# Kernel optimization log

Hardware: AMD Instinct MI355X
Metric: run time of the kernel (lower is better)

## Reference

```python
import jax, jax.numpy as jnp
import numpy as np

N_NODES = 358
NODE_DIM = 64
EMBED_DIM = 96
G_HEADS = 4
TOPK = 10
B = 8
P = 72
MHA_HEADS = 4


def _ln(x, g, b, eps=1e-5):
    m = x.mean(-1, keepdims=True)
    v = jnp.var(x, axis=-1, keepdims=True)
    return (x - m) * jax.lax.rsqrt(v + eps) * g + b


def _gelu(x):
    return jax.nn.gelu(x, approximate=False)


def _topk_sparsify(a, k):
    # top-k mask per row over last dim, then row-renormalize (matches torch version)
    shp = a.shape
    n = shp[-1]
    flat = a.reshape(-1, n)
    _, idx = jax.lax.top_k(flat, k)
    rows = jnp.arange(flat.shape[0])[:, None]
    mask = jnp.zeros_like(flat).at[rows, idx].set(1.0)
    sp = flat * mask
    sp = sp / (sp.sum(-1, keepdims=True) + 1e-8)
    return sp.reshape(shp)


def _forward(patch_features, se2, le1, le2, ge1, ge2, temperature, in_proj_w, in_proj_b, out_proj_w, out_proj_b, tn_g, tn_b, de_w1, de_b1, de_ln1_g, de_ln1_b, de_w2, de_b2, de_ln2_g, de_ln2_b, pos_enc, gnn1_w, gnn1_b, gnn1_g, gnn1_beta, gnn2_w, gnn2_b, gnn2_g, gnn2_beta, gf_w, gf_b, ee_w1, ee_b1, ee_ln_g, ee_ln_b, ee_w2, ee_b2, ee_w3, ee_b3):
    Bn, N, Pn, D = patch_features.shape
    H = temperature.shape[0]
    Hl = H // 2
    # --- static multi-head graphs (local + global) ---
    ladj = jax.nn.relu(jnp.einsum('hnd,hdm->hnm', le1, le2))
    ladj = jax.nn.softmax(ladj / jnp.clip(temperature[:Hl] * 2.0, 0.1, 5.0)[:, None, None], axis=-1)
    gadj = jax.nn.relu(jnp.einsum('hnd,hdm->hnm', ge1, ge2))
    gadj = jax.nn.softmax(gadj / jnp.clip(temperature[Hl:] * 0.5, 0.1, 2.0)[:, None, None], axis=-1)
    static_adjs = jnp.concatenate([ladj, gadj], axis=0)  # (H,N,N)
    # --- dynamic graphs from patch features ---
    pr = patch_features.reshape(Bn * N, Pn, D)
    x = pr + pos_enc[:, :Pn, :]
    # torch nn.MultiheadAttention self-attention (eval mode, no dropout)
    qkv = x @ in_proj_w.T + in_proj_b
    q, k, v = jnp.split(qkv, 3, axis=-1)
    hd = D // MHA_HEADS

    def split_heads(t):
        return t.reshape(Bn * N, Pn, MHA_HEADS, hd).transpose(0, 2, 1, 3)

    q, k, v = split_heads(q), split_heads(k), split_heads(v)
    attn = jax.nn.softmax(jnp.einsum('bhqd,bhkd->bhqk', q, k) * (1.0 / float(np.sqrt(hd))), axis=-1)
    att = jnp.einsum('bhqk,bhkd->bhqd', attn, v).transpose(0, 2, 1, 3).reshape(Bn * N, Pn, D)
    att = att @ out_proj_w.T + out_proj_b
    imp = jax.nn.softmax(att.mean(-1), axis=1)  # (BN,P) patch importance
    node_repr = _ln((att * imp[..., None]).sum(1) + pr.mean(1), tn_g, tn_b).reshape(Bn, N, D)
    # dynamic encoder: Linear -> LN -> GELU -> Linear -> LN
    de = _ln(_gelu(_ln(node_repr @ de_w1.T + de_b1, de_ln1_g, de_ln1_b)) @ de_w2.T + de_b2, de_ln2_g, de_ln2_b)
    # two GNN refinement layers: bmm -> softmax -> bmm -> (Linear,LN,GELU) + residual
    for w, b_, g_, bt in ((gnn1_w, gnn1_b, gnn1_g, gnn1_beta), (gnn2_w, gnn2_b, gnn2_g, gnn2_beta)):
        sims = jax.nn.softmax(jnp.einsum('bnd,bmd->bnm', de, de) / 0.2, axis=2)
        agg = jnp.einsum('bnm,bmd->bnd', sims, de)
        de = _gelu(_ln(agg @ w.T + b_, g_, bt)) + de
    dyn = jax.nn.relu(jnp.einsum('bnd,hdm->bhnm', de, se2))
    dynamic_adjs = jax.nn.softmax(dyn / jnp.clip(temperature, 0.1, 2.0)[None, :, None, None], axis=3)
    # --- top-k sparsification ---
    static_adjs = _topk_sparsify(static_adjs, TOPK)
    dynamic_adjs = _topk_sparsify(dynamic_adjs, TOPK)
    # --- static/dynamic fusion ---
    fw = jax.nn.sigmoid(patch_features.mean(2) @ gf_w.T + gf_b)  # (B,N,H)
    fw = fw.transpose(0, 2, 1)[..., None]  # (B,H,N,1) broadcasts over last N
    fused = (1.0 - fw) * static_adjs[None] + fw * dynamic_adjs  # (B,H,N,N)
    # --- edge encoder over head dim ---
    mh = fused.transpose(0, 2, 3, 1)  # (B,N,N,H)
    h1 = _gelu(_ln(mh @ ee_w1.T + ee_b1, ee_ln_g, ee_ln_b))
    h2 = _gelu(h1 @ ee_w2.T + ee_b2)
    ew = (h2 @ ee_w3.T + ee_b3)[..., 0]  # (B,N,N)
    final_adjs = jax.nn.sigmoid(ew) * fused.mean(1)
    return final_adjs, static_adjs, dynamic_adjs


def setup_inputs() -> dict:
    key = jax.random.key(0)
    ks = iter(jax.random.split(key, 64))
    D, nd, H = EMBED_DIM, NODE_DIM, G_HEADS
    Hl = H // 2
    Hg = H - Hl

    def rn(shape, s=0.05):
        return jax.random.normal(next(ks), shape, jnp.float32) * s

    z = lambda *s: jnp.zeros(s, jnp.float32)
    o = lambda *s: jnp.ones(s, jnp.float32)
    return dict(
        patch_features=jax.random.normal(next(ks), (B, N_NODES, P, D), jnp.float32),
        se2=rn((H, nd, N_NODES)),
        le1=rn((Hl, N_NODES, nd // 2)), le2=rn((Hl, nd // 2, N_NODES)),
        ge1=rn((Hg, N_NODES, nd)), ge2=rn((Hg, nd, N_NODES)),
        temperature=jnp.full((H,), 0.5, jnp.float32),
        in_proj_w=rn((3 * D, D)), in_proj_b=z(3 * D),
        out_proj_w=rn((D, D)), out_proj_b=z(D),
        tn_g=o(D), tn_b=z(D),
        de_w1=rn((2 * nd, D)), de_b1=z(2 * nd), de_ln1_g=o(2 * nd), de_ln1_b=z(2 * nd),
        de_w2=rn((nd, 2 * nd)), de_b2=z(nd), de_ln2_g=o(nd), de_ln2_b=z(nd),
        pos_enc=rn((1, 72, D), 1.0),
        gnn1_w=rn((nd, nd)), gnn1_b=z(nd), gnn1_g=o(nd), gnn1_beta=z(nd),
        gnn2_w=rn((nd, nd)), gnn2_b=z(nd), gnn2_g=o(nd), gnn2_beta=z(nd),
        gf_w=rn((H, D)), gf_b=z(H),
        ee_w1=rn((4 * H, H)), ee_b1=z(4 * H), ee_ln_g=o(4 * H), ee_ln_b=z(4 * H),
        ee_w2=rn((2 * H, 4 * H)), ee_b2=z(2 * H),
        ee_w3=rn((1, 2 * H)), ee_b3=z(1),
    )


def reference(patch_features, se2, le1, le2, ge1, ge2, temperature, in_proj_w, in_proj_b, out_proj_w, out_proj_b, tn_g, tn_b, de_w1, de_b1, de_ln1_g, de_ln1_b, de_w2, de_b2, de_ln2_g, de_ln2_b, pos_enc, gnn1_w, gnn1_b, gnn1_g, gnn1_beta, gnn2_w, gnn2_b, gnn2_g, gnn2_beta, gf_w, gf_b, ee_w1, ee_b1, ee_ln_g, ee_ln_b, ee_w2, ee_b2, ee_w3, ee_b3):
    return _forward(patch_features, se2, le1, le2, ge1, ge2, temperature, in_proj_w, in_proj_b, out_proj_w, out_proj_b, tn_g, tn_b, de_w1, de_b1, de_ln1_g, de_ln1_b, de_w2, de_b2, de_ln2_g, de_ln2_b, pos_enc, gnn1_w, gnn1_b, gnn1_g, gnn1_beta, gnn2_w, gnn2_b, gnn2_g, gnn2_beta, gf_w, gf_b, ee_w1, ee_b1, ee_ln_g, ee_ln_b, ee_w2, ee_b2, ee_w3, ee_b3)
```

## Files before the change

kernel.cpp:

```cpp
#include <hip/hip_runtime.h>
#include <math.h>

#define NNODES 358
#define NN2 (358*358)
#define DIM 96
#define PP 72
#define ND 64
#define NB 8
#define NH 4
#define SEQ (NB*NNODES)

#define WS_WT2   0
#define WS_WBAR  27648
#define WS_BBAR  27744
#define WS_POSB  27748
#define WS_PRM   27848
#define WS_DEA   302792
#define WS_DEB   486088

__device__ __forceinline__ float gelu_f(float y) {
  return 0.5f*y*(1.0f+erff(y*0.70710678118654752440f));
}

__device__ __forceinline__ void wave_topk_row(const float* __restrict__ lgr,
                                              float* __restrict__ orow)
{
  int lane = threadIdx.x & 63;
  float vals[6];
  #pragma unroll
  for (int j = 0; j < 6; ++j) {
    int m = lane + 64*j;
    vals[j] = (m < NNODES) ? lgr[m] : -1e30f;
  }
  float mx = vals[0];
  #pragma unroll
  for (int j = 1; j < 6; ++j) mx = fmaxf(mx, vals[j]);
  #pragma unroll
  for (int o = 32; o; o >>= 1) mx = fmaxf(mx, __shfl_xor(mx, o, 64));
  float M = mx;
  float ls = 0.0f;
  #pragma unroll
  for (int j = 0; j < 6; ++j) ls += __expf(vals[j] - M);
  #pragma unroll
  for (int o = 32; o; o >>= 1) ls += __shfl_xor(ls, o, 64);
  float invS = 1.0f/ls;
  float outv[6] = {0.f, 0.f, 0.f, 0.f, 0.f, 0.f};
  float ss = 0.0f;
  for (int it = 0; it < 10; ++it) {
    float v = -1e30f; int idx = 0x7fffffff;
    #pragma unroll
    for (int j = 0; j < 6; ++j) {
      if (vals[j] > v) { v = vals[j]; idx = lane + 64*j; }
    }
    #pragma unroll
    for (int o = 1; o < 64; o <<= 1) {
      float ov = __shfl_xor(v, o, 64);
      int oi = __shfl_xor(idx, o, 64);
      if (ov > v || (ov == v && oi < idx)) { v = ov; idx = oi; }
    }
    ss += __expf(v - M);
    #pragma unroll
    for (int j = 0; j < 6; ++j)
      if (lane + 64*j == idx) { outv[j] = __expf(v - M); vals[j] = -1e30f; }
  }
  float dn = 1.0f/(ss*invS + 1e-8f);
  #pragma unroll
  for (int j = 0; j < 6; ++j) {
    int m = lane + 64*j;
    if (m < NNODES) orow[m] = outv[j]*invS*dn;
  }
}

__global__ void k0_setup(const float* __restrict__ wi, const float* __restrict__ wo,
                         const float* __restrict__ bo, const float* __restrict__ pos,
                         float* __restrict__ ws)
{
  int t = threadIdx.x;
  for (int idx = t; idx < 4*96*72; idx += 256) {
    int h = idx / (96*72);
    int r = idx - h*96*72;
    int k = r / 72;
    int gc = r - k*72;
    int g = gc / 24, c = gc - g*24;
    ws[WS_WT2 + idx] = wi[(size_t)(g*96 + h*24 + c)*96 + k];
  }
  if (t < 96) {
    float sm = 0.0f;
    for (int d = 0; d < 96; ++d) sm += wo[d*96 + t];
    ws[WS_WBAR + t] = sm*(1.0f/96.0f);
    float ps = 0.0f;
    for (int p = 0; p < PP; ++p) ps += pos[p*96 + t];
    ws[WS_POSB + t] = ps*(1.0f/72.0f);
  }
  if (t == 0) {
    float sm = 0.0f;
    for (int d = 0; d < 96; ++d) sm += bo[d];
    ws[WS_BBAR] = sm*(1.0f/96.0f);
  }
}

#define K1_RPB 4
#define K1_BPH 90

__global__ void __launch_bounds__(256)
k1_static4(const float* __restrict__ le1, const float* __restrict__ le2,
           const float* __restrict__ ge1, const float* __restrict__ ge2,
           const float* __restrict__ temp, float* __restrict__ outstat)
{
  __shared__ float e1s[K1_RPB][64];
  __shared__ float lg[K1_RPB][NNODES];
  int blk = blockIdx.x, t = threadIdx.x;
  int h = blk / K1_BPH;
  int n0 = (blk - h*K1_BPH)*K1_RPB;
  int nrows = NNODES - n0; if (nrows > K1_RPB) nrows = K1_RPB;
  int kd; const float* e2p; float tau;
  if (h < 2) {
    kd = 32;
    e2p = le2 + (size_t)h*32*NNODES;
    tau = fminf(fmaxf(temp[h]*2.0f, 0.1f), 5.0f);
  } else {
    kd = 64;
    e2p = ge2 + (size_t)(h-2)*64*NNODES;
    tau = fminf(fmaxf(temp[h]*0.5f, 0.1f), 2.0f);
  }
  {
    int r = t >> 6, k = t & 63;
    float v = 0.0f;
    if (r < nrows && k < kd)
      v = (h < 2) ? le1[((size_t)h*NNODES + n0 + r)*32 + k]
                  : ge1[((size_t)(h-2)*NNODES + n0 + r)*64 + k];
    e1s[r][k] = v;
  }
  __syncthreads();
  float itau = 1.0f/tau;
  for (int m = t; m < NNODES; m += 256) {
    float s0=0.f, s1=0.f, s2=0.f, s3=0.f;
    for (int k = 0; k < kd; ++k) {
      float ev = e2p[k*NNODES + m];
      s0 += e1s[0][k]*ev;
      s1 += e1s[1][k]*ev;
      s2 += e1s[2][k]*ev;
      s3 += e1s[3][k]*ev;
    }
    lg[0][m] = fmaxf(s0, 0.0f)*itau;
    lg[1][m] = fmaxf(s1, 0.0f)*itau;
    lg[2][m] = fmaxf(s2, 0.0f)*itau;
    lg[3][m] = fmaxf(s3, 0.0f)*itau;
  }
  __syncthreads();
  int wv = t >> 6;
  if (wv < nrows)
    wave_topk_row(lg[wv], outstat + ((size_t)h*NNODES + n0 + wv)*NNODES);
}

#define A_XS    0
#define A_WH    7200
#define A_SS    7200
#define A_WB    7200
#define A_LIMP  7296
#define A_IMP   7368
#define A_WSUM  7440
#define A_NB    7536
#define A_NR    7632
#define A_H1    7728
#define A_G1    7856
#define A_H2    7984
#define A_PART  12672
#define A_PART2 13184
#define A_QH    14112
#define A_KT    16128
#define A_VT    17952
#define A_PRM   19776
#define A_TOT   19872

__global__ void __launch_bounds__(512, 4)
k2a_fused(const float* __restrict__ pf, const float* __restrict__ pos,
          const float* __restrict__ inb, float* __restrict__ ws,
          const float* __restrict__ wo, const float* __restrict__ bo,
          const float* __restrict__ tng, const float* __restrict__ tnb,
          const float* __restrict__ dw1, const float* __restrict__ db1,
          const float* __restrict__ dg1, const float* __restrict__ dlb1,
          const float* __restrict__ dw2, const float* __restrict__ db2,
          const float* __restrict__ dg2, const float* __restrict__ dlb2)
{
  __shared__ __align__(16) float L[A_TOT];
  int t = threadIdx.x;
  size_t s = blockIdx.x;
  const float* prp = pf + s*(PP*DIM);
  for (int idx = t; idx < 1728; idx += 512) {
    float4 v = ((const float4*)prp)[idx];
    float4 q = ((const float4*)pos)[idx];
    v.x += q.x; v.y += q.y; v.z += q.z; v.w += q.w;
    int p = idx / 24, e4 = idx - p*24;
    *(float4*)&L[A_XS + p*100 + e4*4] = v;
  }
  __syncthreads();
  if (t < DIM) {
    float sm = 0.0f;
    for (int p = 0; p < PP; ++p) sm += L[A_XS + p*100 + t];
    sm = sm*(1.0f/72.0f) - ws[WS_POSB + t];
    L[A_PRM + t] = sm;
    ws[WS_PRM + s*DIM + t] = sm;
  }
  const float SC = 0.20412414523193150f;
  float4 oreg0, oreg1, oreg2, oreg3;
  #pragma unroll
  for (int h = 0; h < NH; ++h) {
    __syncthreads();
    __builtin_amdgcn_sched_barrier(0);
    const float4* wsrc = (const float4*)(ws + WS_WT2 + (size_t)h*6912);
    for (int idx = t; idx < 1728; idx += 512)
      *(float4*)&L[A_WH + idx*4] = wsrc[idx];
    __builtin_amdgcn_sched_barrier(0);
    __syncthreads();
    if (t < 432) {
      int rt = t / 18, ct = t - rt*18;
      int p0 = rt*3, cc0 = ct*4;
      float acc[3][4];
      #pragma unroll
      for (int a = 0; a < 3; ++a)
        { acc[a][0]=0.f; acc[a][1]=0.f; acc[a][2]=0.f; acc[a][3]=0.f; }
      for (int k0 = 0; k0 < 96; k0 += 4) {
        float4 xv[3];
        #pragma unroll
        for (int a = 0; a < 3; ++a) xv[a] = *(const float4*)&L[A_XS + (p0+a)*100 + k0];
        float4 wv[4];
        #pragma unroll
        for (int kk = 0; kk < 4; ++kk) wv[kk] = *(const float4*)&L[A_WH + (k0+kk)*72 + cc0];
        #pragma unroll
        for (int kk = 0; kk < 4; ++kk) {
          #pragma unroll
          for (int a = 0; a < 3; ++a) {
            float xa = ((const float*)&xv[a])[kk];
            acc[a][0] += xa*wv[kk].x;
            acc[a][1] += xa*wv[kk].y;
            acc[a][2] += xa*wv[kk].z;
            acc[a][3] += xa*wv[kk].w;
          }
        }
      }
      int g = cc0 / 24;
      int ch = cc0 - g*24;
      #pragma unroll
      for (int c = 0; c < 4; ++c) {
        float bias = inb[g*96 + h*24 + ch + c];
        #pragma unroll
        for (int a = 0; a < 3; ++a) {
          float v = acc[a][c] + bias;
          int p = p0 + a;
          if (g == 0)      L[A_QH + p*28 + ch + c] = v*SC;
          else if (g == 1) L[A_KT + (ch+c)*76 + p] = v;
          else             L[A_VT + (ch+c)*76 + p] = v;
        }
      }
    }
    __syncthreads();
    for (int tile = t; tile < 648; tile += 512) {
      int pt2 = tile / 18, jt2 = tile - pt2*18;
      int p0 = pt2*2, j0 = jt2*4;
      float a0=0,a1=0,a2=0,a3=0, c0=0,c1=0,c2=0,c3=0;
      #pragma unroll
      for (int d0 = 0; d0 < 24; d0 += 4) {
        float4 q0 = *(const float4*)&L[A_QH + p0*28 + d0];
        float4 q1 = *(const float4*)&L[A_QH + (p0+1)*28 + d0];
        #pragma unroll
        for (int dd = 0; dd < 4; ++dd) {
          float4 kv = *(const float4*)&L[A_KT + (d0+dd)*76 + j0];
          float qa = ((const float*)&q0)[dd];
          float qb = ((const float*)&q1)[dd];
          a0 += qa*kv.x; a1 += qa*kv.y; a2 += qa*kv.z; a3 += qa*kv.w;
          c0 += qb*kv.x; c1 += qb*kv.y; c2 += qb*kv.z; c3 += qb*kv.w;
        }
      }
      *(float4*)&L[A_SS + p0*76 + j0]     = make_float4(a0,a1,a2,a3);
      *(float4*)&L[A_SS + (p0+1)*76 + j0] = make_float4(c0,c1,c2,c3);
    }
    __syncthreads();
    if (t < 288) {
      int r = t >> 2, sg = t & 3, j0 = sg*18;
      const float* row = &L[A_SS + r*76];
      float mx = row[j0];
      for (int j = j0+1; j < j0+18; ++j) mx = fmaxf(mx, row[j]);
      L[A_PART + t] = mx;
    }
    __syncthreads();
    if (t < 288) {
      int r = t >> 2, sg = t & 3, j0 = sg*18;
      int rb = r << 2;
      float M = fmaxf(fmaxf(L[A_PART+rb], L[A_PART+rb+1]),
                      fmaxf(L[A_PART+rb+2], L[A_PART+rb+3]));
      float* row = &L[A_SS + r*76];
      float sm = 0.0f;
      for (int j = j0; j < j0+18; ++j) { float e = __expf(row[j]-M); row[j] = e; sm += e; }
      L[A_PART2 + t] = sm;
    }
    __syncthreads();
    if (t < 432) {
      int p = t / 6, dt = t - (t/6)*6;
      int d0 = dt*4, rb = p << 2;
      float S4 = L[A_PART2+rb]+L[A_PART2+rb+1]+L[A_PART2+rb+2]+L[A_PART2+rb+3];
      float inv = 1.0f/S4;
      float a0=0,a1=0,a2=0,a3=0;
      for (int j0 = 0; j0 < 72; j0 += 4) {
        float4 pv = *(const float4*)&L[A_SS + p*76 + j0];
        float4 v0 = *(const float4*)&L[A_VT + (d0+0)*76 + j0];
        float4 v1 = *(const float4*)&L[A_VT + (d0+1)*76 + j0];
        float4 v2 = *(const float4*)&L[A_VT + (d0+2)*76 + j0];
        float4 v3 = *(const float4*)&L[A_VT + (d0+3)*76 + j0];
        a0 += pv.x*v0.x + pv.y*v0.y + pv.z*v0.z + pv.w*v0.w;
        a1 += pv.x*v1.x + pv.y*v1.y + pv.z*v1.z + pv.w*v1.w;
        a2 += pv.x*v2.x + pv.y*v2.y + pv.z*v2.z + pv.w*v2.w;
        a3 += pv.x*v3.x + pv.y*v3.y + pv.z*v3.z + pv.w*v3.w;
      }
      float4 ov = make_float4(a0*inv, a1*inv, a2*inv, a3*inv);
      if (h == 0)      oreg0 = ov;
      else if (h == 1) oreg1 = ov;
      else if (h == 2) oreg2 = ov;
      else             oreg3 = ov;
    }
  }
  __syncthreads();
  if (t < 432) {
    int p = t / 6, dt = t - (t/6)*6;
    int d0 = dt*4;
    *(float4*)&L[A_XS + p*100 +  0 + d0] = oreg0;
    *(float4*)&L[A_XS + p*100 + 24 + d0] = oreg1;
    *(float4*)&L[A_XS + p*100 + 48 + d0] = oreg2;
    *(float4*)&L[A_XS + p*100 + 72 + d0] = oreg3;
  }
  if (t < 96) L[A_WB + t] = ws[WS_WBAR + t];
  __syncthreads();
  if (t < 288) {
    int r = t >> 2, sg = t & 3, e0 = sg*24;
    float sm = 0.0f;
    for (int e = e0; e < e0+24; ++e) sm += L[A_XS + r*100 + e]*L[A_WB + e];
    L[A_PART + t] = sm;
  }
  __syncthreads();
  if (t < 72) {
    int rb = t << 2;
    L[A_LIMP + t] = L[A_PART+rb]+L[A_PART+rb+1]+L[A_PART+rb+2]+L[A_PART+rb+3]
                  + ws[WS_BBAR];
  }
  __syncthreads();
  if (t < 72) {
    float mx = L[A_LIMP];
    for (int j = 1; j < 72; ++j) mx = fmaxf(mx, L[A_LIMP+j]);
    float sm = 0.0f;
    for (int j = 0; j < 72; ++j) sm += __expf(L[A_LIMP+j]-mx);
    L[A_IMP + t] = __expf(L[A_LIMP+t]-mx)/sm;
  }
  __syncthreads();
  if (t < 384) {
    int c = t >> 2, sg = t & 3, p0 = sg*18;
    float sm = 0.0f;
    for (int p = p0; p < p0+18; ++p) sm += L[A_IMP+p]*L[A_XS + p*100 + c];
    L[A_PART + t] = sm;
  }
  __syncthreads();
  if (t < 96) {
    int rb = t << 2;
    L[A_WSUM + t] = L[A_PART+rb]+L[A_PART+rb+1]+L[A_PART+rb+2]+L[A_PART+rb+3];
  }
  __syncthreads();
  if (t < 384) {
    int c = t >> 2, sg = t & 3, e0 = sg*24;
    float sm = 0.0f;
    for (int e = e0; e < e0+24; ++e) sm += L[A_WSUM+e]*wo[c*96 + e];
    L[A_PART + t] = sm;
  }
  __syncthreads();
  if (t < 96) {
    int rb = t << 2;
    L[A_NB + t] = L[A_PART+rb]+L[A_PART+rb+1]+L[A_PART+rb+2]+L[A_PART+rb+3]
                + bo[t] + L[A_PRM + t];
  }
  __syncthreads();
  if (t < 96) {
    float mean = 0.0f;
    for (int e = 0; e < 96; ++e) mean += L[A_NB+e];
    mean *= (1.0f/96.0f);
    float var = 0.0f;
    for (int e = 0; e < 96; ++e) { float d = L[A_NB+e]-mean; var += d*d; }
    var *= (1.0f/96.0f);
    L[A_NR + t] = (L[A_NB+t]-mean)*rsqrtf(var+1e-5f)*tng[t] + tnb[t];
  }
  __syncthreads();
  {
    int c = t >> 2, sg = t & 3, k0 = sg*24;
    float sm = 0.0f;
    for (int k = k0; k < k0+24; ++k) sm += L[A_NR+k]*dw1[c*96 + k];
    L[A_PART + t] = sm;
  }
  __syncthreads();
  if (t < 128) {
    int rb = t << 2;
    L[A_H1 + t] = L[A_PART+rb]+L[A_PART+rb+1]+L[A_PART+rb+2]+L[A_PART+rb+3] + db1[t];
  }
  __syncthreads();
  if (t < 128) {
    float mean = 0.0f; for (int e = 0; e < 128; ++e) mean += L[A_H1+e];
    mean *= (1.0f/128.0f);
    float var = 0.0f; for (int e = 0; e < 128; ++e) { float d = L[A_H1+e]-mean; var += d*d; }
    var *= (1.0f/128.0f);
    float y = (L[A_H1+t]-mean)*rsqrtf(var+1e-5f)*dg1[t] + dlb1[t];
    L[A_G1 + t] = gelu_f(y);
  }
  __syncthreads();
  if (t < 256) {
    int c = t >> 2, sg = t & 3, k0 = sg*32;
    float sm = 0.0f;
    for (int k = k0; k < k0+32; ++k) sm += L[A_G1+k]*dw2[c*128 + k];
    L[A_PART + t] = sm;
  }
  __syncthreads();
  if (t < 64) {
    int rb = t << 2;
    L[A_H2 + t] = L[A_PART+rb]+L[A_PART+rb+1]+L[A_PART+rb+2]+L[A_PART+rb+3] + db2[t];
  }
  __syncthreads();
  if (t < 64) {
    float mean = 0.0f; for (int e = 0; e < 64; ++e) mean += L[A_H2+e];
    mean *= (1.0f/64.0f);
    float var = 0.0f; for (int e = 0; e < 64; ++e) { float d = L[A_H2+e]-mean; var += d*d; }
    var *= (1.0f/64.0f);
    ws[WS_DEA + s*ND + t] = (L[A_H2+t]-mean)*rsqrtf(var+1e-5f)*dg2[t] + dlb2[t];
  }
}

#define K4_RPB 4
#define K4_BPB 90

__global__ void __launch_bounds__(256)
k4_gnn(float* __restrict__ ws, int inoff, int outoff,
       const float* __restrict__ w, const float* __restrict__ bb,
       const float* __restrict__ g, const float* __restrict__ beta)
{
  __shared__ __align__(16) float nrow[K4_RPB][64];
  __shared__ float lg[K4_RPB][NNODES];
  __shared__ float pbl[K4_RPB][NNODES];
  __shared__ float aggp[4][K4_RPB][64];
  __shared__ float aggb[K4_RPB][64];
  __shared__ float prj[K4_RPB][64];
  int blk = blockIdx.x, t = threadIdx.x;
  int b = blk / K4_BPB;
  int n0 = (blk - b*K4_BPB)*K4_RPB;
  int nrows = NNODES - n0; if (nrows > K4_RPB) nrows = K4_RPB;
  {
    int r = t >> 6, d = t & 63;
    nrow[r][d] = (r < nrows)
      ? ws[inoff + ((size_t)(b*NNODES) + n0 + r)*ND + d] : 0.0f;
  }
  __syncthreads();
  const float* deb = ws + inoff + (size_t)b*NNODES*ND;
  for (int m = t; m < NNODES; m += 256) {
    const float* dr = deb + (size_t)m*ND;
    float s0=0.f, s1=0.f, s2=0.f, s3=0.f;
    #pragma unroll
    for (int d0 = 0; d0 < 64; d0 += 4) {
      float4 dv = *(const float4*)&dr[d0];
      float4 n0v = *(const float4*)&nrow[0][d0];
      float4 n1v = *(const float4*)&nrow[1][d0];
      float4 n2v = *(const float4*)&nrow[2][d0];
      float4 n3v = *(const float4*)&nrow[3][d0];
      s0 += dv.x*n0v.x + dv.y*n0v.y + dv.z*n0v.z + dv.w*n0v.w;
      s1 += dv.x*n1v.x + dv.y*n1v.y + dv.z*n1v.z + dv.w*n1v.w;
      s2 += dv.x*n2v.x + dv.y*n2v.y + dv.z*n2v.z + dv.w*n2v.w;
      s3 += dv.x*n3v.x + dv.y*n3v.y + dv.z*n3v.z + dv.w*n3v.w;
    }
    lg[0][m] = s0*5.0f;
    lg[1][m] = s1*5.0f;
    lg[2][m] = s2*5.0f;
    lg[3][m] = s3*5.0f;
  }
  __syncthreads();
  int wv = t >> 6, lane = t & 63;
  {
    const float* lgr = lg[wv];
    float vals[6];
    #pragma unroll
    for (int j = 0; j < 6; ++j) {
      int m = lane + 64*j;
      vals[j] = (m < NNODES) ? lgr[m] : -1e30f;
    }
    float mx = vals[0];
    #pragma unroll
    for (int j = 1; j < 6; ++j) mx = fmaxf(mx, vals[j]);
    #pragma unroll
    for (int o = 32; o; o >>= 1) mx = fmaxf(mx, __shfl_xor(mx, o, 64));
    float M = mx;
    float ls = 0.0f;
    #pragma unroll
    for (int j = 0; j < 6; ++j) ls += __expf(vals[j] - M);
    #pragma unroll
    for (int o = 32; o; o >>= 1) ls += __shfl_xor(ls, o, 64);
    float inv = 1.0f/ls;
    #pragma unroll
    for (int j = 0; j < 6; ++j) {
      int m = lane + 64*j;
      if (m < NNODES) pbl[wv][m] = __expf(vals[j] - M)*inv;
    }
  }
  __syncthreads();
  {
    int d = lane;
    float a0=0.f, a1=0.f, a2=0.f, a3=0.f;
    for (int m = wv; m < NNODES; m += 4) {
      float dv = deb[(size_t)m*ND + d];
      a0 += pbl[0][m]*dv;
      a1 += pbl[1][m]*dv;
      a2 += pbl[2][m]*dv;
      a3 += pbl[3][m]*dv;
    }
    aggp[wv][0][d] = a0;
    aggp[wv][1][d] = a1;
    aggp[wv][2][d] = a2;
    aggp[wv][3][d] = a3;
  }
  __syncthreads();
  {
    int r = t >> 6, d = t & 63;
    aggb[r][d] = aggp[0][r][d]+aggp[1][r][d]+aggp[2][r][d]+aggp[3][r][d];
  }
  __syncthreads();
  {
    int r = t >> 6, c = t & 63;
    float sm = 0.0f;
    for (int d = 0; d < 64; ++d) sm += aggb[r][d]*w[c*64 + d];
    prj[r][c] = sm + bb[c];
  }
  __syncthreads();
  {
    int r = t >> 6, c = t & 63;
    float mean = 0.0f; for (int e = 0; e < 64; ++e) mean += prj[r][e];
    mean *= (1.0f/64.0f);
    float var = 0.0f; for (int e = 0; e < 64; ++e) { float d = prj[r][e]-mean; var += d*d; }
    var *= (1.0f/64.0f);
    float y = (prj[r][c]-mean)*rsqrtf(var+1e-5f)*g[c] + beta[c];
    if (r < nrows)
      ws[outoff + ((size_t)(b*NNODES) + n0 + r)*ND + c] = gelu_f(y) + nrow[r][c];
  }
}

#define K5_RPB 4
#define K5_BPH 90

__global__ void __launch_bounds__(256)
k5_dyn4(const float* __restrict__ ws, const float* __restrict__ se2,
        const float* __restrict__ temp, float* __restrict__ outdyn)
{
  __shared__ float den[K5_RPB][64];
  __shared__ float lg[K5_RPB][NNODES];
  int blk = blockIdx.x, t = threadIdx.x;
  int bh = blk / K5_BPH;
  int n0 = (blk - bh*K5_BPH)*K5_RPB;
  int h = bh & 3, b = bh >> 2;
  int nrows = NNODES - n0; if (nrows > K5_RPB) nrows = K5_RPB;
  if (t < K5_RPB*64) {
    int r = t >> 6, d = t & 63;
    den[r][d] = (r < nrows)
      ? ws[WS_DEA + ((size_t)(b*NNODES) + n0 + r)*ND + d] : 0.0f;
  }
  __syncthreads();
  float tau = fminf(fmaxf(temp[h], 0.1f), 2.0f);
  const float* sp = se2 + (size_t)h*64*NNODES;
  float itau = 1.0f/tau;
  for (int m = t; m < NNODES; m += 256) {
    float s0=0.f, s1=0.f, s2=0.f, s3=0.f;
    for (int d = 0; d < 64; ++d) {
      float wv_ = sp[d*NNODES + m];
      s0 += den[0][d]*wv_;
      s1 += den[1][d]*wv_;
      s2 += den[2][d]*wv_;
      s3 += den[3][d]*wv_;
    }
    lg[0][m] = fmaxf(s0, 0.0f)*itau;
    lg[1][m] = fmaxf(s1, 0.0f)*itau;
    lg[2][m] = fmaxf(s2, 0.0f)*itau;
    lg[3][m] = fmaxf(s3, 0.0f)*itau;
  }
  __syncthreads();
  int wv = t >> 6;
  if (wv < nrows)
    wave_topk_row(lg[wv], outdyn + ((size_t)bh*NNODES + n0 + wv)*NNODES);
}

__global__ void __launch_bounds__(256)
k6_fuse(const float* __restrict__ ws, const float* __restrict__ outstat,
        const float* __restrict__ outdyn,
        const float* __restrict__ gfw, const float* __restrict__ gfb,
        const float* __restrict__ ew1, const float* __restrict__ eb1,
        const float* __restrict__ elg, const float* __restrict__ elb,
        const float* __restrict__ ew2, const float* __restrict__ eb2,
        const float* __restrict__ ew3, const float* __restrict__ eb3,
        float* __restrict__ outfin)
{
  __shared__ float sw1[64], sb1[16], slg[16], slb[16], sw2[128], sb2[8], sw3[8], sb3[1], sfw[4];
  int blk = blockIdx.x, t = threadIdx.x;
  int b = blk / NNODES, n = blk - b*NNODES;
  if (t < 64)  sw1[t] = ew1[t];
  if (t < 16)  { sb1[t] = eb1[t]; slg[t] = elg[t]; slb[t] = elb[t]; }
  if (t < 128) sw2[t] = ew2[t];
  if (t < 8)   { sb2[t] = eb2[t]; sw3[t] = ew3[t]; }
  if (t == 0)  sb3[0] = eb3[0];
  if (t < 4) {
    const float* pm = ws + WS_PRM + (size_t)blk*DIM;
    float sm = gfb[t];
    for (int e = 0; e < DIM; ++e) sm += pm[e]*gfw[t*DIM + e];
    sfw[t] = 1.0f/(1.0f+__expf(-sm));
  }
  __syncthreads();
  size_t srow = (size_t)n*NNODES;
  for (int m = t; m < NNODES; m += 256) {
    float fu[4]; float mn = 0.0f;
    #pragma unroll
    for (int hh = 0; hh < 4; ++hh) {
      float sv = outstat[(size_t)hh*NN2 + srow + m];
      float dv = outdyn[((size_t)(b*4+hh)*NNODES + n)*NNODES + m];
      float f = (1.0f - sfw[hh])*sv + sfw[hh]*dv;
      fu[hh] = f; mn += f;
    }
    mn *= 0.25f;
    float h1[16]; float m1 = 0.0f;
    #pragma unroll
    for (int j = 0; j < 16; ++j) {
      float sm = sb1[j];
      #pragma unroll
      for (int c = 0; c < 4; ++c) sm += fu[c]*sw1[j*4+c];
      h1[j] = sm; m1 += sm;
    }
    m1 *= (1.0f/16.0f);
    float v1 = 0.0f;
    #pragma unroll
    for (int j = 0; j < 16; ++j) { float d = h1[j]-m1; v1 += d*d; }
    float is1 = rsqrtf(v1*(1.0f/16.0f) + 1e-5f);
    #pragma unroll
    for (int j = 0; j < 16; ++j) h1[j] = gelu_f((h1[j]-m1)*is1*slg[j] + slb[j]);
    float h2[8];
    #pragma unroll
    for (int i = 0; i < 8; ++i) {
      float sm = sb2[i];
      #pragma unroll
      for (int j = 0; j < 16; ++j) sm += h1[j]*sw2[i*16+j];
      h2[i] = gelu_f(sm);
    }
    float ewv = sb3[0];
    #pragma unroll
    for (int i = 0; i < 8; ++i) ewv += h2[i]*sw3[i];
    float fin = (1.0f/(1.0f+__expf(-ewv)))*mn;
    outfin[(size_t)b*NN2 + srow + m] = fin;
  }
}

extern "C" void kernel_launch(void* const* d_in, const int* in_sizes, int n_in,
                              void* d_out, int out_size, void* d_ws, size_t ws_size,
                              hipStream_t stream)
{
  const float* pf   = (const float*)d_in[0];
  const float* se2  = (const float*)d_in[1];
  const float* le1  = (const float*)d_in[2];
  const float* le2  = (const float*)d_in[3];
  const float* ge1  = (const float*)d_in[4];
  const float* ge2  = (const float*)d_in[5];
  const float* temp = (const float*)d_in[6];
  const float* wi   = (const float*)d_in[7];
  const float* inb  = (const float*)d_in[8];
  const float* wo   = (const float*)d_in[9];
  const float* bo   = (const float*)d_in[10];
  const float* tng  = (const float*)d_in[11];
  const float* tnb  = (const float*)d_in[12];
  const float* dw1  = (const float*)d_in[13];
  const float* db1  = (const float*)d_in[14];
  const float* dg1  = (const float*)d_in[15];
  const float* dlb1 = (const float*)d_in[16];
  const float* dw2  = (const float*)d_in[17];
  const float* db2  = (const float*)d_in[18];
  const float* dg2  = (const float*)d_in[19];
  const float* dlb2 = (const float*)d_in[20];
  const float* pos  = (const float*)d_in[21];
  const float* g1w  = (const float*)d_in[22];
  const float* g1b  = (const float*)d_in[23];
  const float* g1g  = (const float*)d_in[24];
  const float* g1be = (const float*)d_in[25];
  const float* g2w  = (const float*)d_in[26];
  const float* g2b  = (const float*)d_in[27];
  const float* g2g  = (const float*)d_in[28];
  const float* g2be = (const float*)d_in[29];
  const float* gfw  = (const float*)d_in[30];
  const float* gfb  = (const float*)d_in[31];
  const float* ew1  = (const float*)d_in[32];
  const float* eb1  = (const float*)d_in[33];
  const float* elg  = (const float*)d_in[34];
  const float* elb  = (const float*)d_in[35];
  const float* ew2  = (const float*)d_in[36];
  const float* eb2  = (const float*)d_in[37];
  const float* ew3  = (const float*)d_in[38];
  const float* eb3  = (const float*)d_in[39];
  float* ws = (float*)d_ws;
  float* out = (float*)d_out;
  float* outfin  = out;
  float* outstat = out + (size_t)NB*NN2;
  float* outdyn  = out + (size_t)(NB+NH)*NN2;

  k0_setup<<<1, 256, 0, stream>>>(wi, wo, bo, pos, ws);
  k1_static4<<<NH*K1_BPH, 256, 0, stream>>>(le1, le2, ge1, ge2, temp, outstat);
  k2a_fused<<<SEQ, 512, 0, stream>>>(pf, pos, inb, ws, wo, bo, tng, tnb,
                                     dw1, db1, dg1, dlb1, dw2, db2, dg2, dlb2);
  k4_gnn<<<NB*K4_BPB, 256, 0, stream>>>(ws, WS_DEA, WS_DEB, g1w, g1b, g1g, g1be);
  k4_gnn<<<NB*K4_BPB, 256, 0, stream>>>(ws, WS_DEB, WS_DEA, g2w, g2b, g2g, g2be);
  k5_dyn4<<<NB*NH*K5_BPH, 256, 0, stream>>>(ws, se2, temp, outdyn);
  k6_fuse<<<SEQ, 256, 0, stream>>>(ws, outstat, outdyn, gfw, gfb,
                                   ew1, eb1, elg, elb, ew2, eb2, ew3, eb3, outfin);
}
```

Measured before the change: 916.6 us.

## Enlarge per-thread register tiles in attention matmuls and fuse softmax via shuffles

Per-head QKV projection, QK^T and PV loops now compute larger register tiles per thread (4x6, 4x4, 2x4), so fewer threads work but each reuses loaded LDS values more. The two-pass softmax max/sum reduction through LDS partials is replaced by wave shuffles, which removes one barrier and an LDS round trip per head. This cuts LDS traffic and synchronisation in exchange for fewer active threads and higher register pressure, which may lower occupancy or parallelism.

```diff
diff --git a/kernel.cpp b/kernel.cpp
--- a/kernel.cpp
+++ b/kernel.cpp
@@ -203,7 +203,7 @@
     ws[WS_PRM + s*DIM + t] = sm;
   }
   const float SC = 0.20412414523193150f;
-  float4 oreg0, oreg1, oreg2, oreg3;
+  float4 o0a, o0b, o1a, o1b, o2a, o2b, o3a, o3b;
   #pragma unroll
   for (int h = 0; h < NH; ++h) {
     __syncthreads();
@@ -213,39 +213,40 @@
       *(float4*)&L[A_WH + idx*4] = wsrc[idx];
     __builtin_amdgcn_sched_barrier(0);
     __syncthreads();
-    if (t < 432) {
-      int rt = t / 18, ct = t - rt*18;
-      int p0 = rt*3, cc0 = ct*4;
-      float acc[3][4];
+    if (t < 216) {
+      int rt = t / 12, ct = t - rt*12;
+      int p0 = rt*4, gc0 = ct*6;
+      float acc[4][6];
       #pragma unroll
-      for (int a = 0; a < 3; ++a)
-        { acc[a][0]=0.f; acc[a][1]=0.f; acc[a][2]=0.f; acc[a][3]=0.f; }
+      for (int a = 0; a < 4; ++a)
+        #pragma unroll
+        for (int c = 0; c < 6; ++c) acc[a][c] = 0.0f;
       for (int k0 = 0; k0 < 96; k0 += 4) {
-        float4 xv[3];
+        float4 xv[4];
         #pragma unroll
-        for (int a = 0; a < 3; ++a) xv[a] = *(const float4*)&L[A_XS + (p0+a)*100 + k0];
-        float4 wv[4];
-        #pragma unroll
-        for (int kk = 0; kk < 4; ++kk) wv[kk] = *(const float4*)&L[A_WH + (k0+kk)*72 + cc0];
+        for (int a = 0; a < 4; ++a) xv[a] = *(const float4*)&L[A_XS + (p0+a)*100 + k0];
+        const float* wr = &L[A_WH + k0*72 + gc0];
         #pragma unroll
         for (int kk = 0; kk < 4; ++kk) {
+          float2 w01 = *(const float2*)(wr + kk*72);
+          float2 w23 = *(const float2*)(wr + kk*72 + 2);
+          float2 w45 = *(const float2*)(wr + kk*72 + 4);
+          float wv[6] = {w01.x, w01.y, w23.x, w23.y, w45.x, w45.y};
           #pragma unroll
-          for (int a = 0; a < 3; ++a) {
+          for (int a = 0; a < 4; ++a) {
             float xa = ((const float*)&xv[a])[kk];
-            acc[a][0] += xa*wv[kk].x;
-            acc[a][1] += xa*wv[kk].y;
-            acc[a][2] += xa*wv[kk].z;
-            acc[a][3] += xa*wv[kk].w;
+            #pragma unroll
+            for (int c = 0; c < 6; ++c) acc[a][c] += xa*wv[c];
           }
         }
       }
-      int g = cc0 / 24;
-      int ch = cc0 - g*24;
+      int g = gc0 / 24;
+      int ch = gc0 - g*24;
       #pragma unroll
-      for (int c = 0; c < 4; ++c) {
+      for (int c = 0; c < 6; ++c) {
         float bias = inb[g*96 + h*24 + ch + c];
         #pragma unroll
-        for (int a = 0; a < 3; ++a) {
+        for (int a = 0; a < 4; ++a) {
           float v = acc[a][c] + bias;
           int p = p0 + a;
           if (g == 0)      L[A_QH + p*28 + ch + c] = v*SC;
@@ -255,78 +256,90 @@
       }
     }
     __syncthreads();
-    for (int tile = t; tile < 648; tile += 512) {
-      int pt2 = tile / 18, jt2 = tile - pt2*18;
-      int p0 = pt2*2, j0 = jt2*4;
-      float a0=0,a1=0,a2=0,a3=0, c0=0,c1=0,c2=0,c3=0;
+    if (t < 324) {
+      int pt = t / 18, jt = t - pt*18;
+      int p0 = pt*4, j0 = jt*4;
+      float acc[4][4];
+      #pragma unroll
+      for (int a = 0; a < 4; ++a)
+        { acc[a][0]=0.f; acc[a][1]=0.f; acc[a][2]=0.f; acc[a][3]=0.f; }
       #pragma unroll
       for (int d0 = 0; d0 < 24; d0 += 4) {
-        float4 q0 = *(const float4*)&L[A_QH + p0*28 + d0];
-        float4 q1 = *(const float4*)&L[A_QH + (p0+1)*28 + d0];
+        float4 q[4];
+        #pragma unroll
+        for (int a = 0; a < 4; ++a) q[a] = *(const float4*)&L[A_QH + (p0+a)*28 + d0];
         #pragma unroll
         for (int dd = 0; dd < 4; ++dd) {
           float4 kv = *(const float4*)&L[A_KT + (d0+dd)*76 + j0];
-          float qa = ((const float*)&q0)[dd];
-          float qb = ((const float*)&q1)[dd];
-          a0 += qa*kv.x; a1 += qa*kv.y; a2 += qa*kv.z; a3 += qa*kv.w;
-          c0 += qb*kv.x; c1 += qb*kv.y; c2 += qb*kv.z; c3 += qb*kv.w;
+          #pragma unroll
+          for (int a = 0; a < 4; ++a) {
+            float qa = ((const float*)&q[a])[dd];
+            acc[a][0] += qa*kv.x;
+            acc[a][1] += qa*kv.y;
+            acc[a][2] += qa*kv.z;
+            acc[a][3] += qa*kv.w;
+          }
         }
       }
-      *(float4*)&L[A_SS + p0*76 + j0]     = make_float4(a0,a1,a2,a3);
-      *(float4*)&L[A_SS + (p0+1)*76 + j0] = make_float4(c0,c1,c2,c3);
+      #pragma unroll
+      for (int a = 0; a < 4; ++a)
+        *(float4*)&L[A_SS + (p0+a)*76 + j0] =
+          make_float4(acc[a][0], acc[a][1], acc[a][2], acc[a][3]);
     }
     __syncthreads();
     if (t < 288) {
       int r = t >> 2, sg = t & 3, j0 = sg*18;
-      const float* row = &L[A_SS + r*76];
+      float* row = &L[A_SS + r*76];
       float mx = row[j0];
       for (int j = j0+1; j < j0+18; ++j) mx = fmaxf(mx, row[j]);
-      L[A_PART + t] = mx;
+      mx = fmaxf(mx, __shfl_xor(mx, 1, 64));
+      mx = fmaxf(mx, __shfl_xor(mx, 2, 64));
+      float sm = 0.0f;
+      for (int j = j0; j < j0+18; ++j) { float e = __expf(row[j]-mx); row[j] = e; sm += e; }
+      sm += __shfl_xor(sm, 1, 64);
+      sm += __shfl_xor(sm, 2, 64);
+      if (sg == 0) L[A_PART2 + r] = sm;
     }
     __syncthreads();
-    if (t < 288) {
-      int r = t >> 2, sg = t & 3, j0 = sg*18;
-      int rb = r << 2;
-      float M = fmaxf(fmaxf(L[A_PART+rb], L[A_PART+rb+1]),
-                      fmaxf(L[A_PART+rb+2], L[A_PART+rb+3]));
-      float* row = &L[A_SS + r*76];
-      float sm = 0.0f;
-      for (int j = j0; j < j0+18; ++j) { float e = __expf(row[j]-M); row[j] = e; sm += e; }
-      L[A_PART2 + t] = sm;
-    }
-    __syncthreads();
-    if (t < 432) {
-      int p = t / 6, dt = t - (t/6)*6;
-      int d0 = dt*4, rb = p << 2;
-      float S4 = L[A_PART2+rb]+L[A_PART2+rb+1]+L[A_PART2+rb+2]+L[A_PART2+rb+3];
-      float inv = 1.0f/S4;
-      float a0=0,a1=0,a2=0,a3=0;
+    if (t < 216) {
+      int pt = t / 6, dt = t - (t/6)*6;
+      int p0 = pt*2, d0 = dt*4;
+      float inv0 = 1.0f/L[A_PART2 + p0];
+      float inv1 = 1.0f/L[A_PART2 + p0 + 1];
+      float acc[2][4];
+      #pragma unroll
+      for (int a = 0; a < 2; ++a)
+        { acc[a][0]=0.f; acc[a][1]=0.f; acc[a][2]=0.f; acc[a][3]=0.f; }
       for (int j0 = 0; j0 < 72; j0 += 4) {
-        float4 pv = *(const float4*)&L[A_SS + p*76 + j0];
-        float4 v0 = *(const float4*)&L[A_VT + (d0+0)*76 + j0];
-        float4 v1 = *(const float4*)&L[A_VT + (d0+1)*76 + j0];
-        float4 v2 = *(const float4*)&L[A_VT + (d0+2)*76 + j0];
-        float4 v3 = *(const float4*)&L[A_VT + (d0+3)*76 + j0];
-        a0 += pv.x*v0.x + pv.y*v0.y + pv.z*v0.z + pv.w*v0.w;
-        a1 += pv.x*v1.x + pv.y*v1.y + pv.z*v1.z + pv.w*v1.w;
-        a2 += pv.x*v2.x + pv.y*v2.y + pv.z*v2.z + pv.w*v2.w;
-        a3 += pv.x*v3.x + pv.y*v3.y + pv.z*v3.z + pv.w*v3.w;
+        float4 pv0 = *(const float4*)&L[A_SS + p0*76 + j0];
+        float4 pv1 = *(const float4*)&L[A_SS + (p0+1)*76 + j0];
+        #pragma unroll
+        for (int dd = 0; dd < 4; ++dd) {
+          float4 vv = *(const float4*)&L[A_VT + (d0+dd)*76 + j0];
+          acc[0][dd] += pv0.x*vv.x + pv0.y*vv.y + pv0.z*vv.z + pv0.w*vv.w;
+          acc[1][dd] += pv1.x*vv.x + pv1.y*vv.y + pv1.z*vv.z + pv1.w*vv.w;
+        }
       }
-      float4 ov = make_float4(a0*inv, a1*inv, a2*inv, a3*inv);
-      if (h == 0)      oreg0 = ov;
-      else if (h == 1) oreg1 = ov;
-      else if (h == 2) oreg2 = ov;
-      else             oreg3 = ov;
-    }
-  }
-  __syncthreads();
-  if (t < 432) {
-    int p = t / 6, dt = t - (t/6)*6;
-    int d0 = dt*4;
-    *(float4*)&L[A_XS + p*100 +  0 + d0] = oreg0;
-    *(float4*)&L[A_XS + p*100 + 24 + d0] = oreg1;
-    *(float4*)&L[A_XS + p*100 + 48 + d0] = oreg2;
-    *(float4*)&L[A_XS + p*100 + 72 + d0] = oreg3;
+      float4 oa = make_float4(acc[0][0]*inv0, acc[0][1]*inv0, acc[0][2]*inv0, acc[0][3]*inv0);
+      float4 ob = make_float4(acc[1][0]*inv1, acc[1][1]*inv1, acc[1][2]*inv1, acc[1][3]*inv1);
+      if (h == 0)      { o0a = oa; o0b = ob; }
+      else if (h == 1) { o1a = oa; o1b = ob; }
+      else if (h == 2) { o2a = oa; o2b = ob; }
+      else             { o3a = oa; o3b = ob; }
+    }
+  }
+  __syncthreads();
+  if (t < 216) {
+    int pt = t / 6, dt = t - (t/6)*6;
+    int p0 = pt*2, d0 = dt*4;
+    *(float4*)&L[A_XS + p0*100     +  0 + d0] = o0a;
+    *(float4*)&L[A_XS + (p0+1)*100 +  0 + d0] = o0b;
+    *(float4*)&L[A_XS + p0*100     + 24 + d0] = o1a;
+    *(float4*)&L[A_XS + (p0+1)*100 + 24 + d0] = o1b;
+    *(float4*)&L[A_XS + p0*100     + 48 + d0] = o2a;
+    *(float4*)&L[A_XS + (p0+1)*100 + 48 + d0] = o2b;
+    *(float4*)&L[A_XS + p0*100     + 72 + d0] = o3a;
+    *(float4*)&L[A_XS + (p0+1)*100 + 72 + d0] = o3b;
   }
   if (t < 96) L[A_WB + t] = ws[WS_WBAR + t];
   __syncthreads();
```

Result: slower. 989.1 us (+7.9%).
